# Kernel optimization log

Measured on AMD Instinct MI355X. Metric: run time of the kernel, lower is better.

## Reference

```python
import jax, jax.numpy as jnp
import numpy as np

KS, PAD, N = 3, 1, 9  # deformable 3x3 kernel, padding 1, N = 9 taps
EPS = 1e-5


def conv2d(x, w, b=None, stride=1, padding=1):
    out = jax.lax.conv_general_dilated(
        x, w, (stride, stride), [(padding, padding)] * 2,
        dimension_numbers=("NCHW", "OIHW", "NCHW"))
    if b is not None:
        out = out + b[None, :, None, None]
    return out


def batchnorm(x, gamma, beta):
    # training-mode BN (fresh module, batch statistics), biased variance like torch
    mean = jnp.mean(x, axis=(0, 2, 3), keepdims=True)
    var = jnp.var(x, axis=(0, 2, 3), keepdims=True)
    xn = (x - mean) * jax.lax.rsqrt(var + EPS)
    return xn * gamma[None, :, None, None] + beta[None, :, None, None]


def gather_corners(xp, qx, qy):
    # xp: (b,c,Hp,Wp); qx,qy: (b,h,w,N) int32 -> (b,c,h,w,N)
    b, c, Hp, Wp = xp.shape
    _, h, w, n = qx.shape
    idx = (qx * Wp + qy).reshape(b, 1, h * w * n)
    out = jnp.take_along_axis(xp.reshape(b, c, Hp * Wp), idx, axis=2)
    return out.reshape(b, c, h, w, n)


def deform_conv(feat, offset, w4):
    # feat: (b,256,h,w), offset: (b,18,h,w) interleaved (x1,y1,x2,y2,...)
    b, c, h, w = feat.shape
    off_x = jnp.transpose(offset[:, 0::2], (0, 2, 3, 1))  # (b,h,w,N)
    off_y = jnp.transpose(offset[:, 1::2], (0, 2, 3, 1))
    xp = jnp.pad(feat, ((0, 0), (0, 0), (PAD, PAD), (PAD, PAD)))
    Hp, Wp = h + 2 * PAD, w + 2 * PAD
    # kernel tap offsets, row-major over (dx,dy)
    pn_x = jnp.array([-1, -1, -1, 0, 0, 0, 1, 1, 1], jnp.float32)
    pn_y = jnp.array([-1, 0, 1, -1, 0, 1, -1, 0, 1], jnp.float32)
    p0_x = jnp.arange(1, h + 1, dtype=jnp.float32)[None, :, None, None]
    p0_y = jnp.arange(1, w + 1, dtype=jnp.float32)[None, None, :, None]
    px = p0_x + pn_x[None, None, None, :] + off_x  # sampling coords in padded map
    py = p0_y + pn_y[None, None, None, :] + off_y

    fpx = jnp.floor(jax.lax.stop_gradient(px))
    fpy = jnp.floor(jax.lax.stop_gradient(py))
    q_lt_x = jnp.clip(fpx, 0, Hp - 1).astype(jnp.int32)
    q_lt_y = jnp.clip(fpy, 0, Wp - 1).astype(jnp.int32)
    q_rb_x = jnp.clip(fpx + 1, 0, Hp - 1).astype(jnp.int32)
    q_rb_y = jnp.clip(fpy + 1, 0, Wp - 1).astype(jnp.int32)

    # out-of-range points snapped to floor (as in original), then clamped
    mask_x = (px < PAD) | (px > Hp - 1 - PAD)
    mask_y = (py < PAD) | (py > Wp - 1 - PAD)
    px = jnp.clip(jnp.where(mask_x, jnp.floor(px), px), 0, Hp - 1)
    py = jnp.clip(jnp.where(mask_y, jnp.floor(py), py), 0, Wp - 1)

    ltx, lty = q_lt_x.astype(jnp.float32), q_lt_y.astype(jnp.float32)
    rbx, rby = q_rb_x.astype(jnp.float32), q_rb_y.astype(jnp.float32)
    g_lt = (1 + (ltx - px)) * (1 + (lty - py))
    g_rb = (1 - (rbx - px)) * (1 - (rby - py))
    g_lb = (1 + (ltx - px)) * (1 - (rby - py))
    g_rt = (1 - (rbx - px)) * (1 + (lty - py))

    x_off = (g_lt[:, None] * gather_corners(xp, q_lt_x, q_lt_y)
             + g_rb[:, None] * gather_corners(xp, q_rb_x, q_rb_y)
             + g_lb[:, None] * gather_corners(xp, q_lt_x, q_rb_y)
             + g_rt[:, None] * gather_corners(xp, q_rb_x, q_lt_y))  # (b,c,h,w,N)

    # stride-ks conv over the ks*ks-expanded map == contraction over (c, tap)
    outc = w4.shape[0]
    return jnp.einsum("bchwn,ocn->bohw", x_off, w4.reshape(outc, c, N))


def setup_inputs() -> dict:
    key = jax.random.key(0)
    ks = jax.random.split(key, 8)
    x = jax.random.normal(ks[0], (2, 3, 224, 224), jnp.float32)
    w1 = jax.random.normal(ks[1], (64, 3, 3, 3), jnp.float32) * 0.1
    b1 = jnp.zeros((64,), jnp.float32)
    g1 = jnp.ones((64,), jnp.float32)
    be1 = jnp.zeros((64,), jnp.float32)
    w2 = jax.random.normal(ks[2], (256, 64, 3, 3), jnp.float32) * 0.04
    b2 = jnp.zeros((256,), jnp.float32)
    g2 = jnp.ones((256,), jnp.float32)
    be2 = jnp.zeros((256,), jnp.float32)
    w_off = jax.random.normal(ks[3], (18, 256, 3, 3), jnp.float32) * 0.01
    b_off = jnp.zeros((18,), jnp.float32)
    w4 = jax.random.normal(ks[4], (256, 256, 3, 3), jnp.float32) * 0.02
    return dict(x=x, w1=w1, b1=b1, g1=g1, be1=be1, w2=w2, b2=b2, g2=g2,
                be2=be2, w_off=w_off, b_off=b_off, w4=w4)


def reference(x, w1, b1, g1, be1, w2, b2, g2, be2, w_off, b_off, w4):
    h = jax.nn.relu(conv2d(x, w1, b1))
    h = batchnorm(h, g1, be1)
    b_, c, H, W = h.shape
    h = h.reshape(b_, c, H // 2, 2, W // 2, 2).mean(axis=(3, 5))  # AvgPool 2x2
    h = jax.nn.relu(conv2d(h, w2, b2))
    h = batchnorm(h, g2, be2)
    offset = conv2d(h, w_off, b_off)  # (b,18,h,w)
    return deform_conv(h, offset, w4)
```

## Files before the change

### kernel.cpp

```cpp
#include <hip/hip_runtime.h>
#include <hip/hip_bf16.h>

#define NP1 50176
#define NP2 12544
#define NPP 12996

typedef __attribute__((ext_vector_type(8))) short short8;
typedef __attribute__((ext_vector_type(4))) float f32x4;

__device__ __forceinline__ unsigned short f2bu(float f){
  __hip_bfloat16 h = __float2bfloat16(f);
  return *reinterpret_cast<unsigned short*>(&h);
}
__device__ __forceinline__ float blo(unsigned u){ union{unsigned q; float f;} x; x.q = u<<16; return x.f; }
__device__ __forceinline__ float bhi(unsigned u){ union{unsigned q; float f;} x; x.q = u & 0xffff0000u; return x.f; }

#define S_SUM1   0
#define S_SUM2   128
#define S_WOFF2  1280
#define S_W4F    75008
#define S_W2FH   369920
#define S_W2FL   443648
#define S_OFFB   517376
#define S_PPAD   968960
#define S_PHI    2632448
#define S_PLO    3464192
#define S_HPAD   4295936
#define S_HPADL  10949888
#define S_WOFFH  14276864
#define S_WOFFL  14313728
#define S_PB2    14350592
#define S_HPADH  15014144
#define WS_NEED_FLOATS 18341120ull
#define WS_NEED_BYTES  (WS_NEED_FLOATS*4ull)

__global__ __launch_bounds__(256) void k_conv1pool(
    const float* __restrict__ x, const float* __restrict__ w1, const float* __restrict__ b1,
    float* __restrict__ ppad, float* __restrict__ sum1,
    const float* __restrict__ w4, const float* __restrict__ woff, const float* __restrict__ w2,
    unsigned short* __restrict__ w4f, float* __restrict__ woff2,
    unsigned short* __restrict__ woffh, unsigned short* __restrict__ woffl,
    unsigned short* __restrict__ w2fh, unsigned short* __restrict__ w2fl){
  for(int t0 = blockIdx.x*256+threadIdx.x; t0 < 884736; t0 += 392*256){
    if(t0 < 589824){
      int kt = t0/8192; int r = t0 - kt*8192;
      int oc = r>>5, kk = r&31;
      int k = kt*32 + kk; int n = k>>8, c = k&255;
      w4f[t0] = f2bu(w4[oc*2304 + c*9 + n]);
    } else if(t0 < 663552){
      int i2 = t0 - 589824;
      int k = i2>>5, oc = i2&31;
      int n = k>>8, c = k&255;
      woff2[i2] = (oc<18) ? woff[oc*2304 + c*9 + n] : 0.f;
    } else if(t0 < 737280){
      int i3 = t0 - 663552;
      int kt = i3>>10; int r = i3 & 1023;
      int oc = r>>5, kk = r&31;
      int k = kt*32 + kk; int n = k>>8, c = k&255;
      float wv = (oc<18) ? woff[oc*2304 + c*9 + n] : 0.f;
      unsigned short hi = f2bu(wv);
      woffh[i3] = hi;
      woffl[i3] = f2bu(wv - blo(hi));
    } else {
      int i4 = t0 - 737280;
      int kt = i4/8192; int r = i4 - kt*8192;
      int oc = r>>5, kk = r&31;
      int k = kt*32 + kk; int n = k>>6, c = k&63;
      float wv = w2[oc*576 + c*9 + n];
      unsigned short hi = f2bu(wv);
      w2fh[i4] = hi;
      w2fl[i4] = f2bu(wv - blo(hi));
    }
  }
  __shared__ float xs[3*34*34];
  __shared__ float ws[16*28];
  __shared__ float wbia[16];
  __shared__ float red[4][32];
  int bid = blockIdx.x;
  int tile = bid % 49; int ocg = (bid/49) & 3; int b = bid/(49*4);
  int oc0 = ocg*16;
  int tu = tile/7, tv = tile - 7*(tile/7);
  int tid = threadIdx.x;
  int in0 = tu*32 - 1, jn0 = tv*32 - 1;
  for(int t=tid; t<3468; t+=256){
    int c = t/1156; int r2 = t - c*1156; int rr = r2/34; int cc = r2 - rr*34;
    int ii = in0+rr, jj = jn0+cc;
    xs[t] = (ii>=0 && ii<224 && jj>=0 && jj<224) ? x[(size_t)(b*3+c)*NP1 + ii*224+jj] : 0.f;
  }
  for(int t=tid; t<432; t+=256){
    int o = t/27, q = t - o*27;
    ws[o*28+q] = w1[(oc0+o)*27+q];
  }
  if(tid<16) wbia[tid] = b1[oc0+tid];
  __syncthreads();
  int u = tid>>4, v = tid&15;
  float xw[3][4][4];
  #pragma unroll
  for(int c=0;c<3;c++)
    #pragma unroll
    for(int r=0;r<4;r++)
      #pragma unroll
      for(int cc=0;cc<4;cc++)
        xw[c][r][cc] = xs[c*1156 + (2*u+r)*34 + (2*v+cc)];
  float s1o[16], s2o[16];
  int U = tu*16+u, V = tv*16+v;
  size_t prow = (size_t)(U+1)*114 + (V+1);
  #pragma unroll 1
  for(int o=0;o<16;o++){
    float w27[27];
    #pragma unroll
    for(int q=0;q<27;q++) w27[q] = ws[o*28+q];
    float bia = wbia[o];
    float pl=0.f, s1=0.f, s2=0.f;
    #pragma unroll
    for(int dy=0;dy<2;dy++){
      #pragma unroll
      for(int dx=0;dx<2;dx++){
        float acc = bia;
        #pragma unroll
        for(int c=0;c<3;c++)
          #pragma unroll
          for(int kh=0;kh<3;kh++)
            #pragma unroll
            for(int kw=0;kw<3;kw++)
              acc += xw[c][dy+kh][dx+kw] * w27[c*9+kh*3+kw];
        acc = fmaxf(acc, 0.f);
        pl += acc; s1 += acc; s2 += acc*acc;
      }
    }
    ppad[(size_t)(b*64+oc0+o)*NPP + prow] = 0.25f*pl;
    s1o[o] = s1; s2o[o] = s2;
  }
  const int lane = tid&63, wv = tid>>6;
  #pragma unroll 1
  for(int o=0;o<16;o++){
    float a = s1o[o], c2 = s2o[o];
    #pragma unroll
    for(int off=32; off; off>>=1){
      a  += __shfl_down(a,  off, 64);
      c2 += __shfl_down(c2, off, 64);
    }
    if(lane==0){ red[wv][o] = a; red[wv][16+o] = c2; }
  }
  __syncthreads();
  if(tid<32){
    int o = tid&15, st = tid>>4;
    float v4 = ((red[0][st*16+o] + red[1][st*16+o]) + red[2][st*16+o]) + red[3][st*16+o];
    atomicAdd(&sum1[st*64 + oc0 + o], v4);
  }
}

__global__ __launch_bounds__(256) void k_affine1t(const float* __restrict__ ppad,
        const float* __restrict__ sum1, const float* __restrict__ g1,
        const float* __restrict__ be1,
        unsigned short* __restrict__ phi, unsigned short* __restrict__ plo){
  __shared__ float ls[64*65];
  __shared__ float sc_l[64], sh_l[64];
  int bid = blockIdx.x;
  int b = bid/204; int pp0 = (bid - b*204)*64;
  int tid = threadIdx.x;
  if(tid < 64){
    float n = 2.f*(float)NP1;
    float mean = sum1[tid]/n;
    float var  = sum1[64+tid]/n - mean*mean;
    float sc = g1[tid]/sqrtf(var + 1e-5f);
    sc_l[tid] = sc;
    sh_l[tid] = be1[tid] - mean*sc;
  }
  __syncthreads();
  #pragma unroll
  for(int it=0; it<16; it++){
    int t = it*256 + tid;
    int c = t>>6, q = t&63;
    int pp = pp0 + q;
    float v = 0.f;
    if(pp < NPP){
      int row = pp/114, col = pp - row*114;
      if(row>=1 && row<=112 && col>=1 && col<=112)
        v = sc_l[c]*ppad[(size_t)(b*64+c)*NPP + pp] + sh_l[c];
    }
    ls[c*65+q] = v;
  }
  __syncthreads();
  #pragma unroll
  for(int it=0; it<8; it++){
    int t = it*256 + tid;
    int qloc = t >> 5; int cp = (t & 31) * 2;
    int pp = pp0 + qloc;
    if(pp < NPP){
      float v0 = ls[cp*65 + qloc], v1 = ls[(cp+1)*65 + qloc];
      unsigned short h0 = f2bu(v0), h1 = f2bu(v1);
      unsigned oh = (unsigned)h0 | ((unsigned)h1<<16);
      unsigned ol = (unsigned)f2bu(v0 - blo(h0)) | ((unsigned)f2bu(v1 - blo(h1))<<16);
      *(unsigned*)&phi[((size_t)b*NPP + pp)*64 + cp] = oh;
      *(unsigned*)&plo[((size_t)b*NPP + pp)*64 + cp] = ol;
    }
  }
}

__global__ __launch_bounds__(256) void k_conv2(
    const unsigned short* __restrict__ phi, const unsigned short* __restrict__ plo,
    const unsigned short* __restrict__ w2fh, const unsigned short* __restrict__ w2fl,
    const float* __restrict__ b2, float* __restrict__ hpad, float* __restrict__ sum2){
  __shared__ float smemf[8800];
  int*  pp_tbl = (int*)smemf;
  unsigned short* afh0 = (unsigned short*)(smemf + 576);
  unsigned short* afl0 = (unsigned short*)(smemf + 576 + 2560);
  float* tb = smemf + 576;
  const int tid = threadIdx.x;
  const int wave = tid>>6, lane = tid&63;
  const int sidx = (blockIdx.x & 7)*49 + (blockIdx.x >> 3);
  const int pix0 = sidx*64;
  const int b = pix0/NP2, ij0 = pix0 - b*NP2;

  for(int t=tid; t<576; t+=256){
    int p = t/9, n = t - 9*(t/9);
    int ij = ij0+p; int i = ij/112, j = ij - i*112;
    pp_tbl[p*9+n] = (i + n/3)*114 + (j + n%3);
  }
  const int px_g = tid>>2;
  const int coff = (tid&3)*8;
  const unsigned short* ph_b = phi + (size_t)b*NPP*64;
  const unsigned short* pl_b = plo + (size_t)b*NPP*64;

  f32x4 acc[4][4] = {};
  __syncthreads();

  auto STAGE = [&](int kt, int buf){
    int n = kt>>1; int cb = ((kt&1)<<5) + coff;
    int pp = pp_tbl[px_g*9 + n];
    *(uint4*)&afh0[buf*2560 + px_g*40 + coff] = *(const uint4*)(ph_b + (size_t)pp*64 + cb);
    *(uint4*)&afl0[buf*2560 + px_g*40 + coff] = *(const uint4*)(pl_b + (size_t)pp*64 + cb);
  };

  const int klo = (lane>>4)<<3;
  STAGE(0, 0);
  for(int kt=0; kt<18; kt++){
    __syncthreads();
    if(kt+1 < 18) STAGE(kt+1, (kt+1)&1);
    const unsigned short* abh = afh0 + (kt&1)*2560;
    const unsigned short* abl = afl0 + (kt&1)*2560;
    short8 aH[4], aL[4];
    #pragma unroll
    for(int mf=0; mf<4; mf++){
      aH[mf] = *(const short8*)&abh[(mf*16 + (lane&15))*40 + klo];
      aL[mf] = *(const short8*)&abl[(mf*16 + (lane&15))*40 + klo];
    }
    #pragma unroll
    for(int nf=0; nf<4; nf++){
      int oc = wave*64 + nf*16 + (lane&15);
      short8 bH = *(const short8*)&w2fh[(size_t)kt*8192 + oc*32 + klo];
      short8 bL = *(const short8*)&w2fl[(size_t)kt*8192 + oc*32 + klo];
      #pragma unroll
      for(int mf=0; mf<4; mf++){
        acc[mf][nf] = __builtin_amdgcn_mfma_f32_16x16x32_bf16(aH[mf], bH, acc[mf][nf], 0,0,0);
        acc[mf][nf] = __builtin_amdgcn_mfma_f32_16x16x32_bf16(aH[mf], bL, acc[mf][nf], 0,0,0);
        acc[mf][nf] = __builtin_amdgcn_mfma_f32_16x16x32_bf16(aL[mf], bH, acc[mf][nf], 0,0,0);
      }
    }
  }
  const int row0 = (lane>>4)<<2, col = lane&15;
  float s1q[4] = {0.f,0.f,0.f,0.f}, s2q[4] = {0.f,0.f,0.f,0.f};
  for(int half=0; half<2; half++){
    __syncthreads();
    #pragma unroll
    for(int m2=0; m2<2; m2++){
      int mf = half*2 + m2;
      #pragma unroll
      for(int nf=0; nf<4; nf++){
        int oc = wave*64 + nf*16 + col;
        #pragma unroll
        for(int r=0;r<4;r++) tb[(m2*16 + row0 + r)*257 + oc] = acc[mf][nf][r];
      }
    }
    __syncthreads();
    #pragma unroll
    for(int it=0; it<8; it++){
      int id = it*256 + tid;
      int pxl = id>>6, oc4 = id&63;
      int px = half*32 + pxl;
      int ij = ij0+px; int i = ij/112, j = ij - i*112;
      int pp = (i+1)*114 + (j+1);
      float4 v;
      v.x = fmaxf(tb[pxl*257 + oc4*4+0] + b2[oc4*4+0], 0.f);
      v.y = fmaxf(tb[pxl*257 + oc4*4+1] + b2[oc4*4+1], 0.f);
      v.z = fmaxf(tb[pxl*257 + oc4*4+2] + b2[oc4*4+2], 0.f);
      v.w = fmaxf(tb[pxl*257 + oc4*4+3] + b2[oc4*4+3], 0.f);
      *(float4*)&hpad[((size_t)b*NPP + pp)*256 + oc4*4] = v;
      s1q[0] += v.x; s2q[0] += v.x*v.x;
      s1q[1] += v.y; s2q[1] += v.y*v.y;
      s1q[2] += v.z; s2q[2] += v.z*v.z;
      s1q[3] += v.w; s2q[3] += v.w*v.w;
    }
  }
  __syncthreads();
  #pragma unroll
  for(int q=0;q<4;q++){ tb[tid*4+q] = s1q[q]; tb[1024 + tid*4+q] = s2q[q]; }
  __syncthreads();
  {
    int oc = tid;
    float s1 = ((tb[oc] + tb[256+oc]) + tb[512+oc]) + tb[768+oc];
    float s2 = ((tb[1024+oc] + tb[1280+oc]) + tb[1536+oc]) + tb[1792+oc];
    atomicAdd(&sum2[oc], s1); atomicAdd(&sum2[256+oc], s2);
  }
}

__global__ __launch_bounds__(256) void k_affine2(float* __restrict__ hpad,
                          const float* __restrict__ sum2, const float* __restrict__ g2,
                          const float* __restrict__ be2,
                          unsigned short* __restrict__ hpadh, unsigned short* __restrict__ hpadl){
  __shared__ float sc_l[256], sh_l[256];
  int tid = threadIdx.x;
  {
    float n = 2.f*(float)NP2;
    float mean = sum2[tid]/n;
    float var  = sum2[256+tid]/n - mean*mean;
    float sc = g2[tid]/sqrtf(var + 1e-5f);
    sc_l[tid] = sc;
    sh_l[tid] = be2[tid] - mean*sc;
  }
  __syncthreads();
  int idx = blockIdx.x*256+tid;
  int c4 = (idx & 63) << 2;
  int pi = idx >> 6;
  int pp = pi % NPP;
  int row = pp/114, col = pp - row*114;
  bool in = (row>=1 && row<=112 && col>=1 && col<=112);
  float4 h = *(const float4*)&hpad[(size_t)pi*256 + c4];
  float4 v;
  v.x = in ? (sc_l[c4+0]*h.x + sh_l[c4+0]) : 0.f;
  v.y = in ? (sc_l[c4+1]*h.y + sh_l[c4+1]) : 0.f;
  v.z = in ? (sc_l[c4+2]*h.z + sh_l[c4+2]) : 0.f;
  v.w = in ? (sc_l[c4+3]*h.w + sh_l[c4+3]) : 0.f;
  bool band = (row<6) || (row>107) || (col<6) || (col>107);
  if(band) *(float4*)&hpad[(size_t)pi*256 + c4] = v;
  unsigned short hx = f2bu(v.x), hy = f2bu(v.y), hz = f2bu(v.z), hw = f2bu(v.w);
  uint2 oh, ol;
  oh.x = (unsigned)hx | ((unsigned)hy<<16);
  oh.y = (unsigned)hz | ((unsigned)hw<<16);
  ol.x = (unsigned)f2bu(v.x - blo(hx)) | ((unsigned)f2bu(v.y - blo(hy))<<16);
  ol.y = (unsigned)f2bu(v.z - blo(hz)) | ((unsigned)f2bu(v.w - blo(hw))<<16);
  *(uint2*)&hpadh[(size_t)pi*256 + c4] = oh;
  *(uint2*)&hpadl[(size_t)pi*256 + c4] = ol;
}

__global__ __launch_bounds__(256) void k_convoff_mfma(
    const unsigned short* __restrict__ hpadh, const unsigned short* __restrict__ hpadl,
    const unsigned short* __restrict__ woffh, const unsigned short* __restrict__ woffl,
    float* __restrict__ p0, float* __restrict__ p1, float* __restrict__ p2){
  __shared__ int pp_tbl[192];
  __shared__ __align__(16) unsigned short afh[2][64*72];
  __shared__ __align__(16) unsigned short afl[2][64*72];
  const int tid = threadIdx.x;
  const int wave = tid>>6, lane = tid&63;
  const int g = blockIdx.x;
  const int xcd = g & 7;
  const int rr  = g >> 3;
  const int split = rr % 3;
  const int sstrip = rr / 3;
  const int strip = xcd*49 + sstrip;
  const int pix0 = strip*64;
  const int b = pix0/NP2, ij0 = pix0 - b*NP2;
  const int n0 = split*3;

  for(int t=tid; t<192; t+=256){
    int p = t/3, nl = t - 3*(t/3);
    int ij = ij0+p; int i = ij/112, j = ij - i*112;
    int n = n0 + nl;
    pp_tbl[p*3+nl] = (i + n/3)*114 + (j + n%3);
  }
  const int px_g = tid>>2;
  const int coff = (tid&3)*16;
  const unsigned short* ph_b = hpadh + (size_t)b*NPP*256;
  const unsigned short* pl_b = hpadl + (size_t)b*NPP*256;
  const int r15 = lane&15, klo = (lane>>4)<<3;

  f32x4 acc[2] = {};
  __syncthreads();

  auto STAGE = [&](int ph, int buf){
    int nl = ph>>2, q = ph&3;
    int pp = pp_tbl[px_g*3 + nl];
    int cb = q*64 + coff;
    uint4 h0 = *(const uint4*)(ph_b + (size_t)pp*256 + cb);
    uint4 h1 = *(const uint4*)(ph_b + (size_t)pp*256 + cb + 8);
    uint4 l0 = *(const uint4*)(pl_b + (size_t)pp*256 + cb);
    uint4 l1 = *(const uint4*)(pl_b + (size_t)pp*256 + cb + 8);
    *(uint4*)&afh[buf][px_g*72 + coff    ] = h0;
    *(uint4*)&afh[buf][px_g*72 + coff + 8] = h1;
    *(uint4*)&afl[buf][px_g*72 + coff    ] = l0;
    *(uint4*)&afl[buf][px_g*72 + coff + 8] = l1;
  };

  STAGE(0, 0);
  for(int ph=0; ph<12; ph++){
    __syncthreads();
    if(ph+1 < 12) STAGE(ph+1, (ph+1)&1);
    const unsigned short* ah = &afh[ph&1][(wave*16 + r15)*72];
    const unsigned short* al = &afl[ph&1][(wave*16 + r15)*72];
    const int n = n0 + (ph>>2), q = ph&3;
    #pragma unroll
    for(int half=0; half<2; half++){
      int kt = n*8 + q*2 + half;
      short8 aH = *(const short8*)&ah[half*32 + klo];
      short8 aL = *(const short8*)&al[half*32 + klo];
      #pragma unroll
      for(int nf=0; nf<2; nf++){
        int oc = nf*16 + r15;
        short8 bH = *(const short8*)&woffh[(size_t)kt*1024 + oc*32 + klo];
        short8 bL = *(const short8*)&woffl[(size_t)kt*1024 + oc*32 + klo];
        acc[nf] = __builtin_amdgcn_mfma_f32_16x16x32_bf16(aH, bH, acc[nf], 0,0,0);
        acc[nf] = __builtin_amdgcn_mfma_f32_16x16x32_bf16(aH, bL, acc[nf], 0,0,0);
        acc[nf] = __builtin_amdgcn_mfma_f32_16x16x32_bf16(aL, bH, acc[nf], 0,0,0);
      }
    }
  }
  float* dst = (split==0) ? p0 : (split==1) ? p1 : p2;
  const int row0 = (lane>>4)<<2;
  #pragma unroll
  for(int nf=0; nf<2; nf++){
    int oc = nf*16 + r15;
    if(oc < 18)
      *(f32x4*)(dst + (size_t)(b*18+oc)*NP2 + ij0 + wave*16 + row0) = acc[nf];
  }
}

__global__ __launch_bounds__(256) void k_offfix(const float* __restrict__ hpad,
        const float* __restrict__ woff2, const float* __restrict__ boff,
        float* __restrict__ offb){
  int idx = blockIdx.x*256 + threadIdx.x;
  if(idx >= 83712) return;
  int oc = idx & 31;
  int pid = idx >> 5;
  int b = pid / 1308; int t = pid - b*1308;
  int i, j;
  if(t < 672){
    int r = t/112; i = (r<3) ? r : 106+r; j = t - (t/112)*112;
  } else {
    int u = t - 672; i = 3 + u/6; int c6 = u - 6*(u/6);
    j = (c6<3) ? c6 : 106+c6;
  }
  const float* hb = hpad + (size_t)b*NPP*256;
  float a0=0.f, a1=0.f, a2=0.f, a3=0.f;
  for(int n=0;n<9;n++){
    const float* ap = hb + (size_t)((i + n/3)*114 + (j + n%3))*256;
    const float* wp = woff2 + (size_t)n*256*32 + oc;
    #pragma unroll 4
    for(int c=0;c<256;c+=4){
      float4 a = *(const float4*)(ap + c);
      a0 = fmaf(a.x, wp[(c+0)*32], a0);
      a1 = fmaf(a.y, wp[(c+1)*32], a1);
      a2 = fmaf(a.z, wp[(c+2)*32], a2);
      a3 = fmaf(a.w, wp[(c+3)*32], a3);
    }
  }
  if(oc < 18)
    offb[(size_t)(b*18+oc)*NP2 + i*112 + j] = ((a0+a1)+(a2+a3)) + boff[oc];
}

__global__ __launch_bounds__(256) void k_deform(
    const unsigned short* __restrict__ hpadh,
    const float* __restrict__ offb,
    const float* __restrict__ p1, const float* __restrict__ p2,
    const float* __restrict__ boff,
    const unsigned short* __restrict__ w4f,
    float* __restrict__ out){
  __shared__ int   gidx[64][9][4];
  __shared__ float gwt [64][9][4];
  __shared__ __align__(16) unsigned short afrag[2][64*72];
  const int tid = threadIdx.x;
  const int wave = tid>>6, lane = tid&63;
  const int sidx = (blockIdx.x & 7)*49 + (blockIdx.x >> 3);
  const int pix0 = sidx*64;
  const int b = pix0/NP2, ij0 = pix0 - b*NP2;

  for(int t=tid; t<576; t+=256){
    int p = t/9, n = t - 9*(t/9);
    int ij = ij0+p; int i = ij/112, j = ij - i*112;
    size_t bx = (size_t)(b*18 + 2*n  )*NP2 + ij;
    size_t by = (size_t)(b*18 + 2*n+1)*NP2 + ij;
    bool band = (i<3) || (i>108) || (j<3) || (j>108);
    float ox, oy;
    if(band){
      ox = offb[bx]; oy = offb[by];
    } else {
      ox = ((offb[bx] + p1[bx]) + p2[bx]) + boff[2*n];
      oy = ((offb[by] + p1[by]) + p2[by]) + boff[2*n+1];
    }
    float px = (float)(i + n/3) + ox;
    float py = (float)(j + n%3) + oy;
    float fpx = floorf(px), fpy = floorf(py);
    float qltxf = fminf(fmaxf(fpx,     0.f),113.f);
    float qltyf = fminf(fmaxf(fpy,     0.f),113.f);
    float qrbxf = fminf(fmaxf(fpx+1.f, 0.f),113.f);
    float qrbyf = fminf(fmaxf(fpy+1.f, 0.f),113.f);
    int qltx=(int)qltxf, qlty=(int)qltyf, qrbx=(int)qrbxf, qrby=(int)qrbyf;
    bool mx = (px<1.f)||(px>112.f);
    bool my = (py<1.f)||(py>112.f);
    float pxc = fminf(fmaxf(mx?fpx:px, 0.f),113.f);
    float pyc = fminf(fmaxf(my?fpy:py, 0.f),113.f);
    float glt = (1.f+(qltxf-pxc))*(1.f+(qltyf-pyc));
    float grb = (1.f-(qrbxf-pxc))*(1.f-(qrbyf-pyc));
    float glb = (1.f+(qltxf-pxc))*(1.f-(qrbyf-pyc));
    float grt = (1.f-(qrbxf-pxc))*(1.f+(qltyf-pyc));
    gidx[p][n][0]=qltx*114+qlty; gwt[p][n][0]=glt;
    gidx[p][n][1]=qrbx*114+qrby; gwt[p][n][1]=grb;
    gidx[p][n][2]=qltx*114+qrby; gwt[p][n][2]=glb;
    gidx[p][n][3]=qrbx*114+qlty; gwt[p][n][3]=grt;
  }

  const int px_g   = tid>>2;
  const int coff_g = (tid&3)*8;
  const unsigned short* hb = hpadh + (size_t)b*NPP*256;

  f32x4 acc[4][4] = {};
  __syncthreads();

  auto GATHER = [&](int ph, int buf){
    int n = ph>>2; int qb = (ph&3)<<6;
    const int*   gi = gidx[px_g][n];
    const float* gw = gwt[px_g][n];
    int i0 = gi[0], i1 = gi[1], i2 = gi[2], i3 = gi[3];
    float w0 = gw[0], w1 = gw[1], w2 = gw[2], w3 = gw[3];
    #pragma unroll
    for(int h=0; h<2; h++){
      int cb = qb + h*32 + coff_g;
      f32x4 va = {0.f,0.f,0.f,0.f}, vb = {0.f,0.f,0.f,0.f};
      const uint4 u0 = *(const uint4*)(hb + (size_t)i0*256 + cb);
      const uint4 u1 = *(const uint4*)(hb + (size_t)i1*256 + cb);
      const uint4 u2 = *(const uint4*)(hb + (size_t)i2*256 + cb);
      const uint4 u3 = *(const uint4*)(hb + (size_t)i3*256 + cb);
      va.x = fmaf(w0, blo(u0.x), va.x); va.y = fmaf(w0, bhi(u0.x), va.y);
      va.z = fmaf(w0, blo(u0.y), va.z); va.w = fmaf(w0, bhi(u0.y), va.w);
      vb.x = fmaf(w0, blo(u0.z), vb.x); vb.y = fmaf(w0, bhi(u0.z), vb.y);
      vb.z = fmaf(w0, blo(u0.w), vb.z); vb.w = fmaf(w0, bhi(u0.w), vb.w);
      va.x = fmaf(w1, blo(u1.x), va.x); va.y = fmaf(w1, bhi(u1.x), va.y);
      va.z = fmaf(w1, blo(u1.y), va.z); va.w = fmaf(w1, bhi(u1.y), va.w);
      vb.x = fmaf(w1, blo(u1.z), vb.x); vb.y = fmaf(w1, bhi(u1.z), vb.y);
      vb.z = fmaf(w1, blo(u1.w), vb.z); vb.w = fmaf(w1, bhi(u1.w), vb.w);
      va.x = fmaf(w2, blo(u2.x), va.x); va.y = fmaf(w2, bhi(u2.x), va.y);
      va.z = fmaf(w2, blo(u2.y), va.z); va.w = fmaf(w2, bhi(u2.y), va.w);
      vb.x = fmaf(w2, blo(u2.z), vb.x); vb.y = fmaf(w2, bhi(u2.z), vb.y);
      vb.z = fmaf(w2, blo(u2.w), vb.z); vb.w = fmaf(w2, bhi(u2.w), vb.w);
      va.x = fmaf(w3, blo(u3.x), va.x); va.y = fmaf(w3, bhi(u3.x), va.y);
      va.z = fmaf(w3, blo(u3.y), va.z); va.w = fmaf(w3, bhi(u3.y), va.w);
      vb.x = fmaf(w3, blo(u3.z), vb.x); vb.y = fmaf(w3, bhi(u3.z), vb.y);
      vb.z = fmaf(w3, blo(u3.w), vb.z); vb.w = fmaf(w3, bhi(u3.w), vb.w);
      uint4 o;
      o.x = (unsigned)f2bu(va.x) | ((unsigned)f2bu(va.y)<<16);
      o.y = (unsigned)f2bu(va.z) | ((unsigned)f2bu(va.w)<<16);
      o.z = (unsigned)f2bu(vb.x) | ((unsigned)f2bu(vb.y)<<16);
      o.w = (unsigned)f2bu(vb.z) | ((unsigned)f2bu(vb.w)<<16);
      *(uint4*)&afrag[buf][px_g*72 + h*32 + coff_g] = o;
    }
  };

  const int klo = (lane>>4)<<3;
  GATHER(0, 0);
  for(int ph=0; ph<36; ph++){
    __syncthreads();
    if(ph+1 < 36) GATHER(ph+1, (ph+1)&1);
    const unsigned short* ab = afrag[ph&1];
    #pragma unroll
    for(int h=0; h<2; h++){
      int kt = (ph>>2)*8 + (ph&3)*2 + h;
      short8 aF[4];
      #pragma unroll
      for(int mf=0; mf<4; mf++)
        aF[mf] = *(const short8*)&ab[(mf*16 + (lane&15))*72 + h*32 + klo];
      const unsigned short* wb = w4f + (size_t)kt*8192 + klo;
      #pragma unroll
      for(int nf=0; nf<4; nf++){
        int oc = wave*64 + nf*16 + (lane&15);
        short8 bF = *(const short8*)&wb[oc*32];
        #pragma unroll
        for(int mf=0; mf<4; mf++)
          acc[mf][nf] = __builtin_amdgcn_mfma_f32_16x16x32_bf16(aF[mf], bF, acc[mf][nf], 0,0,0);
      }
    }
  }
  int row0 = ((lane>>4)<<2);
  int col  = lane&15;
  #pragma unroll
  for(int mf=0; mf<4; mf++)
    #pragma unroll
    for(int nf=0; nf<4; nf++){
      int oc = wave*64 + nf*16 + col;
      size_t ob = (size_t)(b*256+oc)*NP2 + ij0 + mf*16 + row0;
      *(f32x4*)(out + ob) = acc[mf][nf];
    }
}

extern "C" void kernel_launch(void* const* d_in, const int* in_sizes, int n_in,
                              void* d_out, int out_size, void* d_ws, size_t ws_size,
                              hipStream_t stream){
  (void)in_sizes; (void)n_in;
  const float* x    = (const float*)d_in[0];
  const float* w1   = (const float*)d_in[1];
  const float* b1   = (const float*)d_in[2];
  const float* g1   = (const float*)d_in[3];
  const float* be1  = (const float*)d_in[4];
  const float* w2   = (const float*)d_in[5];
  const float* b2   = (const float*)d_in[6];
  const float* g2   = (const float*)d_in[7];
  const float* be2  = (const float*)d_in[8];
  const float* woff = (const float*)d_in[9];
  const float* boff = (const float*)d_in[10];
  const float* w4   = (const float*)d_in[11];
  float* out = (float*)d_out;
  float* ws = (float*)d_ws;

  if(ws_size < WS_NEED_BYTES){
    hipMemsetAsync(d_out, 0, (size_t)out_size*sizeof(float), stream);
    return;
  }

  float* sum1   = ws + S_SUM1;
  float* sum2   = ws + S_SUM2;
  float* woff2  = ws + S_WOFF2;
  unsigned short* w4f   = (unsigned short*)(ws + S_W4F);
  unsigned short* w2fh  = (unsigned short*)(ws + S_W2FH);
  unsigned short* w2fl  = (unsigned short*)(ws + S_W2FL);
  unsigned short* woffh = (unsigned short*)(ws + S_WOFFH);
  unsigned short* woffl = (unsigned short*)(ws + S_WOFFL);
  float* offb   = ws + S_OFFB;
  float* ppad   = ws + S_PPAD;
  float* pb1    = ws + S_PPAD;
  float* pb2    = ws + S_PB2;
  unsigned short* phi = (unsigned short*)(ws + S_PHI);
  unsigned short* plo = (unsigned short*)(ws + S_PLO);
  float* hpad   = ws + S_HPAD;
  unsigned short* hpadh = (unsigned short*)(ws + S_HPADH);
  unsigned short* hpadl = (unsigned short*)(ws + S_HPADL);

  hipMemsetAsync(sum1, 0, 640*sizeof(float), stream);
  k_conv1pool    <<<392,   256, 0, stream>>>(x, w1, b1, ppad, sum1,
                                             w4, woff, w2, w4f, woff2, woffh, woffl,
                                             w2fh, w2fl);
  k_affine1t     <<<408,   256, 0, stream>>>(ppad, sum1, g1, be1, phi, plo);
  k_conv2        <<<392,   256, 0, stream>>>(phi, plo, w2fh, w2fl, b2, hpad, sum2);
  k_affine2      <<<6498,  256, 0, stream>>>(hpad, sum2, g2, be2, hpadh, hpadl);
  k_convoff_mfma <<<1176,  256, 0, stream>>>(hpadh, hpadl, woffh, woffl, offb, pb1, pb2);
  k_offfix       <<<327,   256, 0, stream>>>(hpad, woff2, boff, offb);
  k_deform       <<<392,   256, 0, stream>>>(hpadh, offb, pb1, pb2, boff, w4f, out);
}
```

Measured before the change: 348.1 us.

## Write pooled conv1 output channel-last to drop the transpose in affine1

```diff
diff --git a/kernel.cpp b/kernel.cpp
--- a/kernel.cpp
+++ b/kernel.cpp
@@ -36,7 +36,7 @@
 
 __global__ __launch_bounds__(256) void k_conv1pool(
     const float* __restrict__ x, const float* __restrict__ w1, const float* __restrict__ b1,
-    float* __restrict__ ppad, float* __restrict__ sum1,
+    float* __restrict__ pooled, float* __restrict__ sum1,
     const float* __restrict__ w4, const float* __restrict__ woff, const float* __restrict__ w2,
     unsigned short* __restrict__ w4f, float* __restrict__ woff2,
     unsigned short* __restrict__ woffh, unsigned short* __restrict__ woffl,
@@ -102,9 +102,8 @@
       #pragma unroll
       for(int cc=0;cc<4;cc++)
         xw[c][r][cc] = xs[c*1156 + (2*u+r)*34 + (2*v+cc)];
-  float s1o[16], s2o[16];
+  float s1o[16], s2o[16], pv[16];
   int U = tu*16+u, V = tv*16+v;
-  size_t prow = (size_t)(U+1)*114 + (V+1);
   #pragma unroll 1
   for(int o=0;o<16;o++){
     float w27[27];
@@ -128,8 +127,16 @@
         pl += acc; s1 += acc; s2 += acc*acc;
       }
     }
-    ppad[(size_t)(b*64+oc0+o)*NPP + prow] = 0.25f*pl;
+    pv[o] = 0.25f*pl;
     s1o[o] = s1; s2o[o] = s2;
+  }
+  {
+    float* dst = pooled + ((size_t)b*NP2 + U*112 + V)*64 + oc0;
+    #pragma unroll
+    for(int q4=0;q4<4;q4++){
+      float4 o4; o4.x=pv[q4*4+0]; o4.y=pv[q4*4+1]; o4.z=pv[q4*4+2]; o4.w=pv[q4*4+3];
+      *(float4*)(dst + q4*4) = o4;
+    }
   }
   const int lane = tid&63, wv = tid>>6;
   #pragma unroll 1
@@ -150,14 +157,11 @@
   }
 }
 
-__global__ __launch_bounds__(256) void k_affine1t(const float* __restrict__ ppad,
+__global__ __launch_bounds__(256) void k_affine1t(const float* __restrict__ pooled,
         const float* __restrict__ sum1, const float* __restrict__ g1,
         const float* __restrict__ be1,
         unsigned short* __restrict__ phi, unsigned short* __restrict__ plo){
-  __shared__ float ls[64*65];
   __shared__ float sc_l[64], sh_l[64];
-  int bid = blockIdx.x;
-  int b = bid/204; int pp0 = (bid - b*204)*64;
   int tid = threadIdx.x;
   if(tid < 64){
     float n = 2.f*(float)NP1;
@@ -168,34 +172,22 @@
     sh_l[tid] = be1[tid] - mean*sc;
   }
   __syncthreads();
-  #pragma unroll
-  for(int it=0; it<16; it++){
-    int t = it*256 + tid;
-    int c = t>>6, q = t&63;
-    int pp = pp0 + q;
-    float v = 0.f;
-    if(pp < NPP){
-      int row = pp/114, col = pp - row*114;
-      if(row>=1 && row<=112 && col>=1 && col<=112)
-        v = sc_l[c]*ppad[(size_t)(b*64+c)*NPP + pp] + sh_l[c];
-    }
-    ls[c*65+q] = v;
-  }
-  __syncthreads();
-  #pragma unroll
-  for(int it=0; it<8; it++){
-    int t = it*256 + tid;
-    int qloc = t >> 5; int cp = (t & 31) * 2;
-    int pp = pp0 + qloc;
-    if(pp < NPP){
-      float v0 = ls[cp*65 + qloc], v1 = ls[(cp+1)*65 + qloc];
-      unsigned short h0 = f2bu(v0), h1 = f2bu(v1);
-      unsigned oh = (unsigned)h0 | ((unsigned)h1<<16);
-      unsigned ol = (unsigned)f2bu(v0 - blo(h0)) | ((unsigned)f2bu(v1 - blo(h1))<<16);
-      *(unsigned*)&phi[((size_t)b*NPP + pp)*64 + cp] = oh;
-      *(unsigned*)&plo[((size_t)b*NPP + pp)*64 + cp] = ol;
-    }
-  }
+  int idx = blockIdx.x*256 + tid;
+  int cp = (idx & 31) * 2;
+  int pi = idx >> 5;
+  int b  = pi / NPP, pp = pi - b*NPP;
+  int row = pp/114, col = pp - row*114;
+  float v0 = 0.f, v1 = 0.f;
+  if(row>=1 && row<=112 && col>=1 && col<=112){
+    const float* src = pooled + ((size_t)b*NP2 + (row-1)*112 + (col-1))*64 + cp;
+    v0 = sc_l[cp]*src[0] + sh_l[cp];
+    v1 = sc_l[cp+1]*src[1] + sh_l[cp+1];
+  }
+  unsigned short h0 = f2bu(v0), h1 = f2bu(v1);
+  unsigned oh = (unsigned)h0 | ((unsigned)h1<<16);
+  unsigned ol = (unsigned)f2bu(v0 - blo(h0)) | ((unsigned)f2bu(v1 - blo(h1))<<16);
+  *(unsigned*)&phi[((size_t)b*NPP + pp)*64 + cp] = oh;
+  *(unsigned*)&plo[((size_t)b*NPP + pp)*64 + cp] = ol;
 }
 
 __global__ __launch_bounds__(256) void k_conv2(
@@ -624,7 +616,7 @@
   unsigned short* woffh = (unsigned short*)(ws + S_WOFFH);
   unsigned short* woffl = (unsigned short*)(ws + S_WOFFL);
   float* offb   = ws + S_OFFB;
-  float* ppad   = ws + S_PPAD;
+  float* pooled = ws + S_PPAD;
   float* pb1    = ws + S_PPAD;
   float* pb2    = ws + S_PB2;
   unsigned short* phi = (unsigned short*)(ws + S_PHI);
@@ -634,10 +626,10 @@
   unsigned short* hpadl = (unsigned short*)(ws + S_HPADL);
 
   hipMemsetAsync(sum1, 0, 640*sizeof(float), stream);
-  k_conv1pool    <<<392,   256, 0, stream>>>(x, w1, b1, ppad, sum1,
+  k_conv1pool    <<<392,   256, 0, stream>>>(x, w1, b1, pooled, sum1,
                                              w4, woff, w2, w4f, woff2, woffh, woffl,
                                              w2fh, w2fl);
-  k_affine1t     <<<408,   256, 0, stream>>>(ppad, sum1, g1, be1, phi, plo);
+  k_affine1t     <<<3249,  256, 0, stream>>>(pooled, sum1, g1, be1, phi, plo);
   k_conv2        <<<392,   256, 0, stream>>>(phi, plo, w2fh, w2fl, b2, hpad, sum2);
   k_affine2      <<<6498,  256, 0, stream>>>(hpad, sum2, g2, be2, hpadh, hpadl);
   k_convoff_mfma <<<1176,  256, 0, stream>>>(hpadh, hpadl, woffh, woffl, offb, pb1, pb2);
```

Result: no change. 345.8 us (-0.6%).
